# Kernel tuning notes

Measured on AMD Instinct MI355X. Metric: run time of the kernel, lower is better.

Reference implementation:

```python
import jax, jax.numpy as jnp
import numpy as np


def _gumbel_from_uniform(u):
    # u in (0,1) -> standard Gumbel noise
    u = jnp.clip(u, 1e-6, 1.0 - 1e-6)
    return -jnp.log(-jnp.log(u))


def _lsq(x, s, num_bits):
    # LSQ fake-quant: scale, clamp to signed range, round (STE), rescale.
    Qp = 2 ** (num_bits - 1) - 1
    Qn = -(2 ** (num_bits - 1))
    xs = x / s
    xc = jnp.clip(xs, Qn, Qp)
    xr = xc + jax.lax.stop_gradient(jnp.round(xc) - xc)
    return xr * s


def _hard_gumbel_softmax(logits, g, tau):
    y = jax.nn.softmax((logits + g) / tau, axis=-1)
    hard = jax.nn.one_hot(jnp.argmax(y, axis=-1), y.shape[-1], dtype=y.dtype)
    return hard + y - jax.lax.stop_gradient(y)


def setup_inputs() -> dict:
    key = jax.random.key(0)
    ks = jax.random.split(key, 16)
    B, L, K, N = 32, 1024, 64, 8
    v = jax.random.normal(ks[0], (B, L, K, 2), dtype=jnp.float32)
    H = jax.random.normal(ks[1], (B, L, N, K, 2), dtype=jnp.float32)
    local_snr = jax.random.uniform(ks[2], (B, L, K, 1), dtype=jnp.float32)
    g_demod = _gumbel_from_uniform(jax.random.uniform(ks[3], (B, L, K, 3), dtype=jnp.float32))
    g_channel = _gumbel_from_uniform(jax.random.uniform(ks[4], (B, L, K, 3), dtype=jnp.float32))
    # policy MLP params (in,out layout), kaiming-ish init
    W1 = jax.random.normal(ks[5], (5, 32), dtype=jnp.float32) * (2.0 / 5) ** 0.5
    b1 = jnp.zeros((32,), dtype=jnp.float32)
    W2 = jax.random.normal(ks[6], (32, 32), dtype=jnp.float32) * (2.0 / 32) ** 0.5
    b2 = jnp.zeros((32,), dtype=jnp.float32)
    Wd = jax.random.normal(ks[7], (32, 3), dtype=jnp.float32) * (1.0 / 32) ** 0.5
    bd = jnp.zeros((3,), dtype=jnp.float32)
    Wc = jax.random.normal(ks[8], (32, 3), dtype=jnp.float32) * (1.0 / 32) ** 0.5
    bc = jnp.zeros((3,), dtype=jnp.float32)
    # LSQ step sizes (scalars) matching init_s of the torch module
    s2d = jnp.float32(0.5)
    s4d = jnp.float32(0.1)
    s2c = jnp.float32(0.5)
    s4c = jnp.float32(0.1)
    return dict(v=v, H=H, local_snr=local_snr, g_demod=g_demod, g_channel=g_channel,
                W1=W1, b1=b1, W2=W2, b2=b2, Wd=Wd, bd=bd, Wc=Wc, bc=bc,
                s2d=s2d, s4d=s4d, s2c=s2c, s4c=s4c)


def reference(v, H, local_snr, g_demod, g_channel,
              W1, b1, W2, b2, Wd, bd, Wc, bc, s2d, s4d, s2c, s4c):
    tau = 1.0
    B, L, K, _ = v.shape
    N = H.shape[2]
    # channel power features: sum over antennas and re/im -> (B,L,K)
    h_power = jnp.sum(H * H, axis=(2, 4))
    channel_norm = h_power[..., None]                      # (B,L,K,1)
    avg_power = jnp.broadcast_to(jnp.mean(h_power, axis=1, keepdims=True), (B, L, K))[..., None]
    pin = jnp.concatenate([v[..., 0:1], v[..., 1:2], local_snr, channel_norm, avg_power], axis=-1)  # (B,L,K,5)
    # tiny router MLP
    h = jax.nn.relu(pin @ W1 + b1)
    h = jax.nn.relu(h @ W2 + b2)
    logits_demod = h @ Wd + bd                              # (B,L,K,3)
    logits_channel = h @ Wc + bc
    w_demod = _hard_gumbel_softmax(logits_demod, g_demod, tau)
    w_channel = _hard_gumbel_softmax(logits_channel, g_channel, tau)
    # weighted combine of fake-quantized branches (0-bit branch contributes 0)
    v_q = w_demod[..., 1:2] * _lsq(v, s2d, 2) + w_demod[..., 2:3] * _lsq(v, s4d, 4)
    w_ch = w_channel[:, :, None]                            # (B,L,1,K,3) broadcast over antennas
    H_q = w_ch[..., 1:2] * _lsq(H, s2c, 2) + w_ch[..., 2:3] * _lsq(H, s4c, 4)
    expected_bits_demod = w_demod[..., 1] * 4.0 + w_demod[..., 2] * 8.0
    expected_bits_channel = w_channel[..., 1] * (2.0 * N * 2) + w_channel[..., 2] * (2.0 * N * 4)
    return (v_q, H_q, expected_bits_demod, expected_bits_channel, w_demod, w_channel)
```

## Files before the change

### kernel.cpp

```cpp
#include <hip/hip_runtime.h>

namespace {
constexpr int Bb = 32, Ll = 1024, Kk = 64, Nn = 8;
constexpr int BLK = Bb * Ll * Kk;
constexpr long long HFLOATS = (long long)BLK * Nn * 2;

constexpr long long OFF_VQ  = 0;
constexpr long long OFF_HQ  = (long long)BLK * 2;
constexpr long long OFF_EBD = OFF_HQ + HFLOATS;
constexpr long long OFF_EBC = OFF_EBD + BLK;
constexpr long long OFF_WD  = OFF_EBC + BLK;
constexpr long long OFF_WC  = OFF_WD + (long long)BLK*3;
}

__device__ __forceinline__ float lsq_fwd(float x, float s, float Qn, float Qp) {
    float xs = x / s;
    float xc = fminf(fmaxf(xs, Qn), Qp);
    return rintf(xc) * s;
}

__device__ __forceinline__ void hard_gumbel(float z0, float z1, float z2, float w[3]) {
    int arg = 0; float m = z0;
    if (z1 > m) { m = z1; arg = 1; }
    if (z2 > m) { m = z2; arg = 2; }
    float e0 = expf(z0 - m), e1 = expf(z1 - m), e2 = expf(z2 - m);
    float s  = e0 + e1 + e2;
    float y0 = e0 / s, y1 = e1 / s, y2 = e2 / s;
    w[0] = ((arg == 0 ? 1.0f : 0.0f) + y0) - y0;
    w[1] = ((arg == 1 ? 1.0f : 0.0f) + y1) - y1;
    w[2] = ((arg == 2 ? 1.0f : 0.0f) + y2) - y2;
}

__global__ __launch_bounds__(256) void hpower_kernel(const float* __restrict__ H,
                                                     float* __restrict__ hp) {
    int t  = blockIdx.x * 256 + threadIdx.x;
    int bl = t >> 6;
    int k  = t & 63;
    const float2* Hb = (const float2*)H + (long long)bl * (Nn * Kk) + k;
    double acc = 0.0;
    #pragma unroll
    for (int n = 0; n < Nn; ++n) {
        float2 h = Hb[n * Kk];
        float a = h.x * h.x;
        float b = h.y * h.y;
        acc += (double)a;
        acc += (double)b;
    }
    hp[t] = (float)acc;
}

__global__ __launch_bounds__(256) void avg_kernel(const float* __restrict__ hp,
                                                  float* __restrict__ avg) {
    int b = blockIdx.x;
    int t = threadIdx.x;
    int k = t & 63, ls = t >> 6;
    double acc = 0.0;
    for (int l = ls; l < Ll; l += 4)
        acc += (double)hp[((long long)b * Ll + l) * Kk + k];
    __shared__ double sh[256];
    sh[t] = acc;
    __syncthreads();
    if (t < 64) {
        double s = (sh[t] + sh[t + 64]) + (sh[t + 128] + sh[t + 192]);
        avg[b * Kk + t] = (float)(s * (1.0 / 1024.0));
    }
}

__global__ __launch_bounds__(256) void mlp_kernel(
    const float* __restrict__ v,  const float* __restrict__ snr,
    const float* __restrict__ gd, const float* __restrict__ gc,
    const float* __restrict__ W1, const float* __restrict__ b1,
    const float* __restrict__ W2, const float* __restrict__ b2,
    const float* __restrict__ Wd, const float* __restrict__ bd,
    const float* __restrict__ Wc, const float* __restrict__ bc,
    const float* __restrict__ ps2d, const float* __restrict__ ps4d,
    const float* __restrict__ hp, const float* __restrict__ avg,
    float* __restrict__ out) {
    int idx = blockIdx.x * 256 + threadIdx.x;
    int b   = idx >> 16;
    int k   = idx & 63;

    float2 vv = ((const float2*)v)[idx];
    float p0 = vv.x, p1 = vv.y;
    float p2 = snr[idx];
    float p3 = hp[idx];
    float p4 = avg[(b << 6) | k];

    float h1[32];
    #pragma unroll
    for (int i = 0; i < 32; ++i) {
        float a = b1[i];
        a = fmaf(p0, W1[i],        a);
        a = fmaf(p1, W1[32 + i],   a);
        a = fmaf(p2, W1[64 + i],   a);
        a = fmaf(p3, W1[96 + i],   a);
        a = fmaf(p4, W1[128 + i],  a);
        h1[i] = fmaxf(a, 0.0f);
    }
    float h2[32];
    #pragma unroll
    for (int i = 0; i < 32; ++i) h2[i] = b2[i];
    #pragma unroll
    for (int j = 0; j < 32; ++j) {
        float hj = h1[j];
        #pragma unroll
        for (int i = 0; i < 32; ++i) h2[i] = fmaf(hj, W2[j * 32 + i], h2[i]);
    }
    #pragma unroll
    for (int i = 0; i < 32; ++i) h2[i] = fmaxf(h2[i], 0.0f);
    float ld[3] = { bd[0], bd[1], bd[2] };
    float lc[3] = { bc[0], bc[1], bc[2] };
    #pragma unroll
    for (int j = 0; j < 32; ++j) {
        float hj = h2[j];
        ld[0] = fmaf(hj, Wd[j * 3 + 0], ld[0]);
        ld[1] = fmaf(hj, Wd[j * 3 + 1], ld[1]);
        ld[2] = fmaf(hj, Wd[j * 3 + 2], ld[2]);
        lc[0] = fmaf(hj, Wc[j * 3 + 0], lc[0]);
        lc[1] = fmaf(hj, Wc[j * 3 + 1], lc[1]);
        lc[2] = fmaf(hj, Wc[j * 3 + 2], lc[2]);
    }

    long long i3 = (long long)idx * 3;
    float wdm[3], wch[3];
    hard_gumbel(ld[0] + gd[i3], ld[1] + gd[i3 + 1], ld[2] + gd[i3 + 2], wdm);
    hard_gumbel(lc[0] + gc[i3], lc[1] + gc[i3 + 1], lc[2] + gc[i3 + 2], wch);

    float s2d = *ps2d, s4d = *ps4d;
    float q0 = wdm[1] * lsq_fwd(p0, s2d, -2.0f, 1.0f) + wdm[2] * lsq_fwd(p0, s4d, -8.0f, 7.0f);
    float q1 = wdm[1] * lsq_fwd(p1, s2d, -2.0f, 1.0f) + wdm[2] * lsq_fwd(p1, s4d, -8.0f, 7.0f);

    ((float2*)(out + OFF_VQ))[idx] = make_float2(q0, q1);
    out[OFF_EBD + idx] = wdm[1] * 4.0f + wdm[2] * 8.0f;
    out[OFF_EBC + idx] = wch[1] * 32.0f + wch[2] * 64.0f;
    out[OFF_WD + i3 + 0] = wdm[0];
    out[OFF_WD + i3 + 1] = wdm[1];
    out[OFF_WD + i3 + 2] = wdm[2];
    out[OFF_WC + i3 + 0] = wch[0];
    out[OFF_WC + i3 + 1] = wch[1];
    out[OFF_WC + i3 + 2] = wch[2];
}

__global__ __launch_bounds__(256) void hq_kernel(const float* __restrict__ H,
                                                 const float* __restrict__ wc,
                                                 const float* __restrict__ ps2c,
                                                 const float* __restrict__ ps4c,
                                                 float* __restrict__ outHQ) {
    long long t = (long long)blockIdx.x * 256 + threadIdx.x;
    float s2c = *ps2c, s4c = *ps4c;
    float2 h = ((const float2*)H)[t];
    int k        = (int)(t & 63);
    long long bl = t >> 9;
    long long wbase = ((bl << 6) | k) * 3;
    float w1 = wc[wbase + 1];
    float w2 = wc[wbase + 2];
    float q0 = w1 * lsq_fwd(h.x, s2c, -2.0f, 1.0f) + w2 * lsq_fwd(h.x, s4c, -8.0f, 7.0f);
    float q1 = w1 * lsq_fwd(h.y, s2c, -2.0f, 1.0f) + w2 * lsq_fwd(h.y, s4c, -8.0f, 7.0f);
    ((float2*)outHQ)[t] = make_float2(q0, q1);
}

extern "C" void kernel_launch(void* const* d_in, const int* in_sizes, int n_in,
                              void* d_out, int out_size, void* d_ws, size_t ws_size,
                              hipStream_t stream) {
    const float* v    = (const float*)d_in[0];
    const float* H    = (const float*)d_in[1];
    const float* snr  = (const float*)d_in[2];
    const float* gd   = (const float*)d_in[3];
    const float* gc   = (const float*)d_in[4];
    const float* W1   = (const float*)d_in[5];
    const float* b1   = (const float*)d_in[6];
    const float* W2   = (const float*)d_in[7];
    const float* b2   = (const float*)d_in[8];
    const float* Wd   = (const float*)d_in[9];
    const float* bd   = (const float*)d_in[10];
    const float* Wc   = (const float*)d_in[11];
    const float* bc   = (const float*)d_in[12];
    const float* s2d  = (const float*)d_in[13];
    const float* s4d  = (const float*)d_in[14];
    const float* s2c  = (const float*)d_in[15];
    const float* s4c  = (const float*)d_in[16];

    float* out = (float*)d_out;
    float* hp  = out + OFF_HQ;
    float* avg = hp + BLK;

    hpower_kernel<<<BLK / 256, 256, 0, stream>>>(H, hp);
    avg_kernel<<<Bb, 256, 0, stream>>>(hp, avg);
    mlp_kernel<<<BLK / 256, 256, 0, stream>>>(v, snr, gd, gc, W1, b1, W2, b2,
                                              Wd, bd, Wc, bc, s2d, s4d, hp, avg, out);
    hq_kernel<<<(int)(HFLOATS / 2 / 256), 256, 0, stream>>>(H, out + OFF_WC, s2c, s4c,
                                                            out + OFF_HQ);
}
```

Before: 537.1 us.

## Fuse H-power, MLP and H quantization into one pass with chunked avg reduction

Replaces the four-kernel pipeline with two kernels. The first computes per-(b,k) channel-power partial sums in 16 L-chunks using 512 blocks instead of 32, without writing the per-element power array. The second loads each H row into registers once, recomputes channel power, runs the MLP and gumbel step, and writes quantized H directly, so the separate hq pass and its re-read of the wc weights go away. H is still read twice, once per kernel, and LSQ division becomes multiplication by a reciprocal, which may change rounding at boundary values.

```diff
diff --git a/kernel.cpp b/kernel.cpp
--- a/kernel.cpp
+++ b/kernel.cpp
@@ -4,6 +4,8 @@
 constexpr int Bb = 32, Ll = 1024, Kk = 64, Nn = 8;
 constexpr int BLK = Bb * Ll * Kk;
 constexpr long long HFLOATS = (long long)BLK * Nn * 2;
+constexpr int CH = 16;
+constexpr int LCH = Ll / CH;
 
 constexpr long long OFF_VQ  = 0;
 constexpr long long OFF_HQ  = (long long)BLK * 2;
@@ -13,9 +15,8 @@
 constexpr long long OFF_WC  = OFF_WD + (long long)BLK*3;
 }
 
-__device__ __forceinline__ float lsq_fwd(float x, float s, float Qn, float Qp) {
-    float xs = x / s;
-    float xc = fminf(fmaxf(xs, Qn), Qp);
+__device__ __forceinline__ float lsq_i(float x, float inv, float s, float Qn, float Qp) {
+    float xc = fminf(fmaxf(x * inv, Qn), Qp);
     return rintf(xc) * s;
 }
 
@@ -31,42 +32,37 @@
     w[2] = ((arg == 2 ? 1.0f : 0.0f) + y2) - y2;
 }
 
-__global__ __launch_bounds__(256) void hpower_kernel(const float* __restrict__ H,
-                                                     float* __restrict__ hp) {
-    int t  = blockIdx.x * 256 + threadIdx.x;
-    int bl = t >> 6;
-    int k  = t & 63;
-    const float2* Hb = (const float2*)H + (long long)bl * (Nn * Kk) + k;
+__global__ __launch_bounds__(256) void hpa_kernel(const float* __restrict__ H,
+                                                  double* __restrict__ partial) {
+    int blk = blockIdx.x;
+    int b   = blk >> 4;
+    int c   = blk & (CH - 1);
+    int t   = threadIdx.x;
+    int k   = t & 63, ls = t >> 6;
+    const float2* Hf = (const float2*)H;
     double acc = 0.0;
-    #pragma unroll
-    for (int n = 0; n < Nn; ++n) {
-        float2 h = Hb[n * Kk];
-        float a = h.x * h.x;
-        float b = h.y * h.y;
-        acc += (double)a;
-        acc += (double)b;
-    }
-    hp[t] = (float)acc;
-}
-
-__global__ __launch_bounds__(256) void avg_kernel(const float* __restrict__ hp,
-                                                  float* __restrict__ avg) {
-    int b = blockIdx.x;
-    int t = threadIdx.x;
-    int k = t & 63, ls = t >> 6;
-    double acc = 0.0;
-    for (int l = ls; l < Ll; l += 4)
-        acc += (double)hp[((long long)b * Ll + l) * Kk + k];
+    int l0 = c * LCH + ls;
+    for (int i = 0; i < LCH / 4; ++i) {
+        int l = l0 + i * 4;
+        const float2* Hb = Hf + (long long)(b * Ll + l) * (Nn * Kk) + k;
+        double e = 0.0;
+        #pragma unroll
+        for (int n = 0; n < Nn; ++n) {
+            float2 h = Hb[n * Kk];
+            e += (double)(h.x * h.x);
+            e += (double)(h.y * h.y);
+        }
+        acc += (double)(float)e;
+    }
     __shared__ double sh[256];
     sh[t] = acc;
     __syncthreads();
-    if (t < 64) {
-        double s = (sh[t] + sh[t + 64]) + (sh[t + 128] + sh[t + 192]);
-        avg[b * Kk + t] = (float)(s * (1.0 / 1024.0));
-    }
-}
-
-__global__ __launch_bounds__(256) void mlp_kernel(
+    if (t < 64)
+        partial[(long long)blk * 64 + t] =
+            (sh[t] + sh[t + 64]) + (sh[t + 128] + sh[t + 192]);
+}
+
+__global__ __launch_bounds__(256) void fused_kernel(
     const float* __restrict__ v,  const float* __restrict__ snr,
     const float* __restrict__ gd, const float* __restrict__ gc,
     const float* __restrict__ W1, const float* __restrict__ b1,
@@ -74,27 +70,47 @@
     const float* __restrict__ Wd, const float* __restrict__ bd,
     const float* __restrict__ Wc, const float* __restrict__ bc,
     const float* __restrict__ ps2d, const float* __restrict__ ps4d,
-    const float* __restrict__ hp, const float* __restrict__ avg,
+    const float* __restrict__ ps2c, const float* __restrict__ ps4c,
+    const double* __restrict__ partial,
+    const float* __restrict__ H,
     float* __restrict__ out) {
     int idx = blockIdx.x * 256 + threadIdx.x;
     int b   = idx >> 16;
     int k   = idx & 63;
+    int bl  = idx >> 6;
+
+    const float2* Hf = (const float2*)H + (long long)bl * (Nn * Kk) + k;
+    float2 hreg[Nn];
+    #pragma unroll
+    for (int n = 0; n < Nn; ++n) hreg[n] = Hf[n * Kk];
+
+    double hacc = 0.0;
+    #pragma unroll
+    for (int n = 0; n < Nn; ++n) {
+        hacc += (double)(hreg[n].x * hreg[n].x);
+        hacc += (double)(hreg[n].y * hreg[n].y);
+    }
+    float p3 = (float)hacc;
+
+    const double* pb = partial + (long long)b * (CH * 64) + k;
+    double s = 0.0;
+    #pragma unroll
+    for (int c = 0; c < CH; ++c) s += pb[c * 64];
+    float p4 = (float)(s * (1.0 / 1024.0));
 
     float2 vv = ((const float2*)v)[idx];
     float p0 = vv.x, p1 = vv.y;
     float p2 = snr[idx];
-    float p3 = hp[idx];
-    float p4 = avg[(b << 6) | k];
 
     float h1[32];
     #pragma unroll
     for (int i = 0; i < 32; ++i) {
         float a = b1[i];
-        a = fmaf(p0, W1[i],        a);
-        a = fmaf(p1, W1[32 + i],   a);
-        a = fmaf(p2, W1[64 + i],   a);
-        a = fmaf(p3, W1[96 + i],   a);
-        a = fmaf(p4, W1[128 + i],  a);
+        a = fmaf(p0, W1[i],       a);
+        a = fmaf(p1, W1[32 + i],  a);
+        a = fmaf(p2, W1[64 + i],  a);
+        a = fmaf(p3, W1[96 + i],  a);
+        a = fmaf(p4, W1[128 + i], a);
         h1[i] = fmaxf(a, 0.0f);
     }
     float h2[32];
@@ -126,11 +142,15 @@
     hard_gumbel(ld[0] + gd[i3], ld[1] + gd[i3 + 1], ld[2] + gd[i3 + 2], wdm);
     hard_gumbel(lc[0] + gc[i3], lc[1] + gc[i3 + 1], lc[2] + gc[i3 + 2], wch);
 
-    float s2d = *ps2d, s4d = *ps4d;
-    float q0 = wdm[1] * lsq_fwd(p0, s2d, -2.0f, 1.0f) + wdm[2] * lsq_fwd(p0, s4d, -8.0f, 7.0f);
-    float q1 = wdm[1] * lsq_fwd(p1, s2d, -2.0f, 1.0f) + wdm[2] * lsq_fwd(p1, s4d, -8.0f, 7.0f);
-
+    float s2d = *ps2d, s4d = *ps4d, s2c = *ps2c, s4c = *ps4c;
+    float i2d = 1.0f / s2d, i4d = 1.0f / s4d, i2c = 1.0f / s2c, i4c = 1.0f / s4c;
+
+    float q0 = wdm[1] * lsq_i(p0, i2d, s2d, -2.0f, 1.0f)
+             + wdm[2] * lsq_i(p0, i4d, s4d, -8.0f, 7.0f);
+    float q1 = wdm[1] * lsq_i(p1, i2d, s2d, -2.0f, 1.0f)
+             + wdm[2] * lsq_i(p1, i4d, s4d, -8.0f, 7.0f);
     ((float2*)(out + OFF_VQ))[idx] = make_float2(q0, q1);
+
     out[OFF_EBD + idx] = wdm[1] * 4.0f + wdm[2] * 8.0f;
     out[OFF_EBC + idx] = wch[1] * 32.0f + wch[2] * 64.0f;
     out[OFF_WD + i3 + 0] = wdm[0];
@@ -139,24 +159,18 @@
     out[OFF_WC + i3 + 0] = wch[0];
     out[OFF_WC + i3 + 1] = wch[1];
     out[OFF_WC + i3 + 2] = wch[2];
-}
-
-__global__ __launch_bounds__(256) void hq_kernel(const float* __restrict__ H,
-                                                 const float* __restrict__ wc,
-                                                 const float* __restrict__ ps2c,
-                                                 const float* __restrict__ ps4c,
-                                                 float* __restrict__ outHQ) {
-    long long t = (long long)blockIdx.x * 256 + threadIdx.x;
-    float s2c = *ps2c, s4c = *ps4c;
-    float2 h = ((const float2*)H)[t];
-    int k        = (int)(t & 63);
-    long long bl = t >> 9;
-    long long wbase = ((bl << 6) | k) * 3;
-    float w1 = wc[wbase + 1];
-    float w2 = wc[wbase + 2];
-    float q0 = w1 * lsq_fwd(h.x, s2c, -2.0f, 1.0f) + w2 * lsq_fwd(h.x, s4c, -8.0f, 7.0f);
-    float q1 = w1 * lsq_fwd(h.y, s2c, -2.0f, 1.0f) + w2 * lsq_fwd(h.y, s4c, -8.0f, 7.0f);
-    ((float2*)outHQ)[t] = make_float2(q0, q1);
+
+    float w1c = wch[1], w2c = wch[2];
+    float2* outHQ = (float2*)(out + OFF_HQ) + (long long)bl * (Nn * Kk) + k;
+    #pragma unroll
+    for (int n = 0; n < Nn; ++n) {
+        float hx = hreg[n].x, hy = hreg[n].y;
+        float qx = w1c * lsq_i(hx, i2c, s2c, -2.0f, 1.0f)
+                 + w2c * lsq_i(hx, i4c, s4c, -8.0f, 7.0f);
+        float qy = w1c * lsq_i(hy, i2c, s2c, -2.0f, 1.0f)
+                 + w2c * lsq_i(hy, i4c, s4c, -8.0f, 7.0f);
+        outHQ[n * Kk] = make_float2(qx, qy);
+    }
 }
 
 extern "C" void kernel_launch(void* const* d_in, const int* in_sizes, int n_in,
@@ -181,13 +195,10 @@
     const float* s4c  = (const float*)d_in[16];
 
     float* out = (float*)d_out;
-    float* hp  = out + OFF_HQ;
-    float* avg = hp + BLK;
-
-    hpower_kernel<<<BLK / 256, 256, 0, stream>>>(H, hp);
-    avg_kernel<<<Bb, 256, 0, stream>>>(hp, avg);
-    mlp_kernel<<<BLK / 256, 256, 0, stream>>>(v, snr, gd, gc, W1, b1, W2, b2,
-                                              Wd, bd, Wc, bc, s2d, s4d, hp, avg, out);
-    hq_kernel<<<(int)(HFLOATS / 2 / 256), 256, 0, stream>>>(H, out + OFF_WC, s2c, s4c,
-                                                            out + OFF_HQ);
-}
+    double* partial = (double*)d_ws;
+
+    hpa_kernel<<<Bb * CH, 256, 0, stream>>>(H, partial);
+    fused_kernel<<<BLK / 256, 256, 0, stream>>>(v, snr, gd, gc, W1, b1, W2, b2,
+                                                Wd, bd, Wc, bc, s2d, s4d, s2c, s4c,
+                                                partial, H, out);
+}
```

Result: faster. 436.7 us (-18.7%).
